# Performance work log

Measured on AMD Instinct MI355X. Metric: run time of the kernel, lower is better.

The kernel has to match this reference:

```python
import jax, jax.numpy as jnp
import numpy as np

EPS = 1e-5  # torch LayerNorm default
H, DH = 8, 64  # heads, dim_head


def _ln(x, g, b):
    mu = jnp.mean(x, axis=-1, keepdims=True)
    var = jnp.var(x, axis=-1, keepdims=True)
    return (x - mu) / jnp.sqrt(var + EPS) * g + b


def setup_inputs() -> dict:
    key = jax.random.key(0)
    ks = jax.random.split(key, 8)
    B, N, M, D, CD = 4, 2048, 256, 1024, 768
    J = M + 1 + N  # context + null + self
    return {
        "x": jax.random.normal(ks[0], (B, N, D), jnp.float32),
        "context": jax.random.normal(ks[1], (B, M, CD), jnp.float32),
        "att_bias": jax.random.normal(ks[2], (B, H, N, J), jnp.float32) * 0.02,
        "ln_g": jnp.ones((D,), jnp.float32),
        "ln_b": jnp.zeros((D,), jnp.float32),
        "null_kv": jax.random.normal(ks[3], (2, DH), jnp.float32),
        "Wq": jax.random.normal(ks[4], (D, H * DH), jnp.float32) * 0.02,
        "Wkv": jax.random.normal(ks[5], (D, 2 * DH), jnp.float32) * 0.02,
        "cln_g": jnp.ones((CD,), jnp.float32),
        "cln_b": jnp.zeros((CD,), jnp.float32),
        "Wc": jax.random.normal(ks[6], (CD, 2 * DH), jnp.float32) * 0.02,
        "bc": jnp.zeros((2 * DH,), jnp.float32),
        "Wo": jax.random.normal(ks[7], (H * DH, D), jnp.float32) * 0.02,
        "oln_g": jnp.ones((D,), jnp.float32),
        "oln_b": jnp.zeros((D,), jnp.float32),
    }


def reference(x, context, att_bias, ln_g, ln_b, null_kv, Wq, Wkv,
              cln_g, cln_b, Wc, bc, Wo, oln_g, oln_b):
    B, N, D = x.shape
    scale = DH ** -0.5
    xn = _ln(x, ln_g, ln_b)
    # queries: per-head [b,h,n,dh], pre-scaled
    q = (xn @ Wq).reshape(B, N, H, DH).transpose(0, 2, 1, 3) * scale
    # shared single-head k/v [b,n,dh]
    kv = xn @ Wkv
    k, v = kv[..., :DH], kv[..., DH:]
    # context k/v [b,m,dh]
    ckv = _ln(context, cln_g, cln_b) @ Wc + bc
    ck, cv = ckv[..., :DH], ckv[..., DH:]
    # null kv token [b,1,dh]
    nk = jnp.broadcast_to(null_kv[0], (B, 1, DH))
    nv = jnp.broadcast_to(null_kv[1], (B, 1, DH))
    # torch order: cat null first, then context -> (ck, nk, k)
    k = jnp.concatenate([ck, nk, k], axis=1)  # [b, j, dh]
    v = jnp.concatenate([cv, nv, v], axis=1)
    score = jnp.einsum('bhid,bjd->bhij', q, k) + att_bias
    probs = jax.nn.softmax(score.astype(jnp.float32), axis=-1).astype(v.dtype)
    att = jnp.einsum('bhij,bjd->bhid', probs, v)
    att = att.transpose(0, 2, 1, 3).reshape(B, N, H * DH)
    return _ln(att @ Wo, oln_g, oln_b)
```

## Files before the change

### kernel.cpp

```cpp
#include <hip/hip_runtime.h>
#include <hip/hip_bf16.h>
#include <cstdint>
#include <cstddef>

#define Bq  4
#define Nq  2048
#define Mq  256
#define Dq  1024
#define CDq 768
#define Hq  8
#define DHq 64
#define Jq  2305
#define QKVN 640
#define NCH 37
#define J2  (NCH * 64)

typedef __bf16  bf16x8 __attribute__((ext_vector_type(8)));
typedef float   f32x4  __attribute__((ext_vector_type(4)));
typedef short   s16x8  __attribute__((ext_vector_type(8)));
typedef unsigned short u16;
typedef unsigned int   u32;

__device__ __forceinline__ u16 f2b(float v) {
  unsigned x = __builtin_bit_cast(unsigned, v);
  unsigned r = (x + 0x7fffu + ((x >> 16) & 1u)) >> 16;
  return (u16)r;
}
__device__ __forceinline__ float b2f(u16 u) {
  unsigned x = ((unsigned)u) << 16;
  return __builtin_bit_cast(float, x);
}
__device__ __forceinline__ u32 cvtpk(float lo, float hi) {
  u32 r;
  asm("v_cvt_pk_bf16_f32 %0, %1, %2" : "=v"(r) : "v"(lo), "v"(hi));
  return r;
}
__device__ __forceinline__ f32x4 mfma16(bf16x8 a, bf16x8 b, f32x4 c) {
  return __builtin_amdgcn_mfma_f32_16x16x32_bf16(a, b, c, 0, 0, 0);
}
__device__ __forceinline__ bf16x8 frag_ld(const u16* p) {
  return __builtin_bit_cast(bf16x8, *(const s16x8*)p);
}
__device__ __forceinline__ void stout(float* p, float v) { *p = v; }
__device__ __forceinline__ void stout(u16*   p, float v) { *p = f2b(v); }

__device__ __forceinline__ void gl_lds16(const void* gSrc, void* ldsDst) {
  __builtin_amdgcn_global_load_lds(
      (const __attribute__((address_space(1))) void*)gSrc,
      (__attribute__((address_space(3))) void*)ldsDst, 16, 0, 0);
}

__global__ __launch_bounds__(256) void prep_kernel(
    const float* __restrict__ x,   const float* __restrict__ ln_g,
    const float* __restrict__ ln_b, u16* __restrict__ xn,
    const float* __restrict__ ctx, const float* __restrict__ cln_g,
    const float* __restrict__ cln_b, u16* __restrict__ ctxn,
    const float* __restrict__ Wq, const float* __restrict__ Wkv,
    const float* __restrict__ Wc, const float* __restrict__ Wo,
    u16* __restrict__ WqkvT, u16* __restrict__ WcT, u16* __restrict__ WoT) {
  const int tid = threadIdx.x;
  if (blockIdx.x < Bq * Nq + Bq * Mq) {
    const int row = blockIdx.x;
    const float* in; const float* g; const float* bb; u16* out; int D;
    if (row < Bq * Nq) {
      in = x + (size_t)row * Dq; g = ln_g; bb = ln_b;
      out = xn + (size_t)row * Dq; D = Dq;
    } else {
      int r2 = row - Bq * Nq;
      in = ctx + (size_t)r2 * CDq; g = cln_g; bb = cln_b;
      out = ctxn + (size_t)r2 * CDq; D = CDq;
    }
    __shared__ float buf[1024];
    __shared__ float red[8];
    float s = 0.f, s2 = 0.f;
    for (int i = tid; i < D; i += 256) {
      float v = in[i];
      buf[i] = v;
      s += v; s2 += v * v;
    }
    #pragma unroll
    for (int off = 32; off; off >>= 1) {
      s  += __shfl_down(s,  off);
      s2 += __shfl_down(s2, off);
    }
    if ((tid & 63) == 0) { red[tid >> 6] = s; red[4 + (tid >> 6)] = s2; }
    __syncthreads();
    float sum = red[0] + red[1] + red[2] + red[3];
    float sq  = red[4] + red[5] + red[6] + red[7];
    float mean = sum / D;
    float var  = sq / D - mean * mean;
    float rstd = rsqrtf(var + 1e-5f);
    for (int i = tid; i < D; i += 256)
      out[i] = f2b((buf[i] - mean) * rstd * g[i] + bb[i]);
  } else {
    __shared__ float T[32][33];
    int bid = blockIdx.x - (Bq * Nq + Bq * Mq);
    const float* W; u16* WT; int K, N, bx, by;
    if (bid < 512)      { W = Wq;  WT = WqkvT;                    K = 1024; N = 512;  bx = bid % 16;        by = bid / 16; }
    else if (bid < 640) { W = Wkv; WT = WqkvT + (size_t)512*1024; K = 1024; N = 128;  bx = (bid-512) % 4;   by = (bid-512) / 4; }
    else if (bid < 736) { W = Wc;  WT = WcT;                      K = 768;  N = 128;  bx = (bid-640) % 4;   by = (bid-640) / 4; }
    else                { W = Wo;  WT = WoT;                      K = 512;  N = 1024; bx = (bid-736) % 32;  by = (bid-736) / 32; }
    const int n0 = bx * 32, k0 = by * 32;
    const int tx = tid & 31, ty = tid >> 5;
    #pragma unroll
    for (int i = 0; i < 32; i += 8)
      T[ty + i][tx] = W[(size_t)(k0 + ty + i) * N + n0 + tx];
    __syncthreads();
    #pragma unroll
    for (int i = 0; i < 32; i += 8)
      WT[(size_t)(n0 + ty + i) * K + k0 + tx] = f2b(T[tx][ty + i]);
  }
}

__global__ __launch_bounds__(256) void ln_out_kernel(
    const float* __restrict__ in, const float* __restrict__ g,
    const float* __restrict__ bb, float* __restrict__ out) {
  const int row = blockIdx.x;
  const int tid = threadIdx.x;
  __shared__ float buf[1024];
  __shared__ float red[8];
  const float* xr = in + (size_t)row * Dq;
  float s = 0.f, s2 = 0.f;
  for (int i = tid; i < Dq; i += 256) {
    float v = xr[i];
    buf[i] = v;
    s += v; s2 += v * v;
  }
  #pragma unroll
  for (int off = 32; off; off >>= 1) {
    s  += __shfl_down(s,  off);
    s2 += __shfl_down(s2, off);
  }
  if ((tid & 63) == 0) { red[tid >> 6] = s; red[4 + (tid >> 6)] = s2; }
  __syncthreads();
  float sum = red[0] + red[1] + red[2] + red[3];
  float sq  = red[4] + red[5] + red[6] + red[7];
  float mean = sum / Dq;
  float var  = sq / Dq - mean * mean;
  float rstd = rsqrtf(var + 1e-5f);
  for (int i = tid; i < Dq; i += 256)
    out[(size_t)row * Dq + i] = (buf[i] - mean) * rstd * g[i] + bb[i];
}

template <typename OT>
__device__ __forceinline__ void gemm_body(const u16* __restrict__ A,
                                          const u16* __restrict__ BT,
                                          OT* __restrict__ C,
                                          int N, int K, int m0, int n0,
                                          u16* Al, u16* Bl) {
  const int tid  = threadIdx.x;
  const int lane = tid & 63, wave = tid >> 6;
  const int l16  = lane & 15, lhi = lane >> 4;
  const int wm = (wave >> 1) * 64, wn = (wave & 1) * 64;

  const int offB = (wave << 10) + (lane << 4);
  const int srow = offB >> 6;
  const int scby = offB & 63;

  f32x4 acc[4][4];
  #pragma unroll
  for (int i = 0; i < 4; ++i)
    #pragma unroll
    for (int j = 0; j < 4; ++j) acc[i][j] = f32x4{0.f, 0.f, 0.f, 0.f};

  for (int k0 = 0; k0 < K; k0 += 32) {
    __syncthreads();
    #pragma unroll
    for (int c = 0; c < 2; ++c) {
      gl_lds16((const char*)(A  + (size_t)(m0 + srow + c * 64) * K + k0) + scby,
               (char*)Al + c * 4096 + (wave << 10));
      gl_lds16((const char*)(BT + (size_t)(n0 + srow + c * 64) * K + k0) + scby,
               (char*)Bl + c * 4096 + (wave << 10));
    }
    __syncthreads();

    bf16x8 af[4], bfr[4];
    #pragma unroll
    for (int mt = 0; mt < 4; ++mt)
      af[mt] = frag_ld(Al + (wm + mt * 16 + l16) * 32 + lhi * 8);
    #pragma unroll
    for (int nt = 0; nt < 4; ++nt)
      bfr[nt] = frag_ld(Bl + (wn + nt * 16 + l16) * 32 + lhi * 8);
    __builtin_amdgcn_s_setprio(1);
    #pragma unroll
    for (int mt = 0; mt < 4; ++mt)
      #pragma unroll
      for (int nt = 0; nt < 4; ++nt)
        acc[mt][nt] = mfma16(af[mt], bfr[nt], acc[mt][nt]);
    __builtin_amdgcn_s_setprio(0);
  }

  #pragma unroll
  for (int mt = 0; mt < 4; ++mt)
    #pragma unroll
    for (int nt = 0; nt < 4; ++nt)
      #pragma unroll
      for (int r = 0; r < 4; ++r)
        stout(C + (size_t)(m0 + wm + mt * 16 + lhi * 4 + r) * N
                + (n0 + wn + nt * 16 + l16),
              acc[mt][nt][r]);
}

__global__ __launch_bounds__(256) void gemm_qkv_ckv(
    const u16* __restrict__ xn, const u16* __restrict__ WqkvT,
    u16* __restrict__ qkv,
    const u16* __restrict__ ctxn, const u16* __restrict__ WcT,
    u16* __restrict__ ckvb) {
  const u16 *A, *BT; u16* C; int N, K, m0, n0;
  if (blockIdx.y < 5) {
    A = xn; BT = WqkvT; C = qkv; N = QKVN; K = Dq;
    m0 = blockIdx.x * 128; n0 = blockIdx.y * 128;
  } else {
    if (blockIdx.x >= 8) return;
    A = ctxn; BT = WcT; C = ckvb; N = 2 * DHq; K = CDq;
    m0 = blockIdx.x * 128; n0 = 0;
  }
  __shared__ __align__(16) u16 Al[128 * 32];
  __shared__ __align__(16) u16 Bl[128 * 32];
  gemm_body<u16>(A, BT, C, N, K, m0, n0, Al, Bl);
}

__global__ __launch_bounds__(256) void gemm128f(const u16* __restrict__ A,
                                                const u16* __restrict__ BT,
                                                float* __restrict__ C,
                                                int N, int K) {
  __shared__ __align__(16) u16 Al[128 * 32];
  __shared__ __align__(16) u16 Bl[128 * 32];
  gemm_body<float>(A, BT, C, N, K, blockIdx.x * 128, blockIdx.y * 128, Al, Bl);
}

__global__ void build_kv(const u16* __restrict__ qkv,
                         const u16* __restrict__ ckvb,
                         const float* __restrict__ nullkv,
                         const float* __restrict__ bc,
                         u16* __restrict__ Kt, u16* __restrict__ Vt) {
  int idx = blockIdx.x * 256 + threadIdx.x;
  if (idx >= Bq * J2 * 64) return;
  int d = idx & 63;
  int t = idx >> 6;
  int j = t % J2;
  int b = t / J2;
  float k = 0.f, v = 0.f;
  if (j < Mq) {
    const u16* p = ckvb + (size_t)(b * Mq + j) * 128;
    k = b2f(p[d])      + bc[d];
    v = b2f(p[64 + d]) + bc[64 + d];
  } else if (j == Mq) {
    k = nullkv[d];
    v = nullkv[64 + d];
  } else if (j < Jq) {
    const u16* p = qkv + (size_t)(b * Nq + (j - Mq - 1)) * QKVN + 512;
    k = b2f(p[d]);
    v = b2f(p[64 + d]);
  }
  int ch = j >> 6, row = j & 63;
  char* tbase = (char*)Kt + ((size_t)(b * NCH + ch)) * 8192;
  *(u16*)(tbase + row * 128 + ((d << 1) ^ ((row & 7) << 4))) = f2b(k);
  char* vbase = (char*)Vt + ((size_t)(b * NCH + ch)) * 8192;
  *(u16*)(vbase + d * 128 + ((row << 1) ^ ((d & 7) << 4))) = f2b(v);
}

__global__ __launch_bounds__(256, 4) void attn_kernel(
    const u16* __restrict__ qkv, const u16* __restrict__ Kt,
    const u16* __restrict__ Vt, const float* __restrict__ bias,
    u16* __restrict__ att) {
  __shared__ __align__(16) u16 Kl [2][4096];
  __shared__ __align__(16) u16 VTl[2][4096];
  __shared__ __align__(16) u16 Pl [4][16][64];
  const int tid  = threadIdx.x;
  const int wave = tid >> 6, lane = tid & 63;
  const int l16  = lane & 15, lhi = lane >> 4;
  const int qt = blockIdx.x, h = blockIdx.y, b = blockIdx.z;
  const int qrow0 = qt * 64 + wave * 16;

  bf16x8 qf[2];
  {
    const u16* qp = qkv + ((size_t)(b * Nq + qrow0 + l16)) * QKVN
                        + h * DHq + lhi * 8;
    qf[0] = frag_ld(qp);
    qf[1] = frag_ld(qp + 32);
  }

  float m_s = -INFINITY, l_s = 0.f;
  f32x4 oacc[4];
  #pragma unroll
  for (int dt = 0; dt < 4; ++dt) oacc[dt] = f32x4{0.f, 0.f, 0.f, 0.f};

  const float* bptr = bias
      + ((size_t)((b * Hq + h) * (size_t)Nq + qrow0 + l16)) * Jq + 4 * lhi;

  const size_t tb0 = (size_t)b * NCH;
  const int soff = (wave << 10) + (lane << 4);
  char* plw = (char*)&Pl[wave][0][0];
  const int pmask = (l16 & 7) << 4;

  auto stage = [&](int buf, int ch) {
    const char* kt = (const char*)Kt + (tb0 + ch) * 8192 + soff;
    const char* vt = (const char*)Vt + (tb0 + ch) * 8192 + soff;
    char* kl = (char*)&Kl[buf][0]  + (wave << 10);
    char* vl = (char*)&VTl[buf][0] + (wave << 10);
    gl_lds16(kt,        kl);
    gl_lds16(kt + 4096, kl + 4096);
    gl_lds16(vt,        vl);
    gl_lds16(vt + 4096, vl + 4096);
  };

  auto loadBias = [&](float (&bv)[4][4], int ch) {
    const int jc = ch * 64;
    if (ch < NCH - 1) {
      #pragma unroll
      for (int jt = 0; jt < 4; ++jt)
        #pragma unroll
        for (int r = 0; r < 4; ++r)
          bv[jt][r] = bptr[jc + 16 * jt + r];
    } else {
      #pragma unroll
      for (int jt = 0; jt < 4; ++jt)
        #pragma unroll
        for (int r = 0; r < 4; ++r) {
          int jg = jc + 16 * jt + 4 * lhi + r;
          bv[jt][r] = (jg < Jq) ? bptr[jc + 16 * jt + r] : -1e30f;
        }
    }
  };

  float bvA[4][4], bvB[4][4];
  stage(0, 0);
  loadBias(bvA, 0);
  __syncthreads();

  auto body = [&](int ch, float (&bvC)[4][4], float (&bvN)[4][4]) {
    const int cur = ch & 1;
    if (ch + 1 < NCH) {
      stage(cur ^ 1, ch + 1);
      loadBias(bvN, ch + 1);
    }

    float sv[4][4];
    __builtin_amdgcn_s_setprio(1);
    #pragma unroll
    for (int jt = 0; jt < 4; ++jt) {
      const int krow = jt * 16 + l16;
      const char* kb = (const char*)&Kl[cur][0] + krow * 128;
      const int sw = (krow & 7) << 4;
      f32x4 s = f32x4{0.f, 0.f, 0.f, 0.f};
      s = mfma16(frag_ld((const u16*)(kb + (((lhi << 4))      ^ sw))), qf[0], s);
      s = mfma16(frag_ld((const u16*)(kb + ((64 + (lhi << 4)) ^ sw))), qf[1], s);
      #pragma unroll
      for (int r = 0; r < 4; ++r)
        sv[jt][r] = s[r] * 0.125f + bvC[jt][r];
    }
    __builtin_amdgcn_s_setprio(0);

    float pmax = sv[0][0];
    #pragma unroll
    for (int jt = 0; jt < 4; ++jt)
      #pragma unroll
      for (int r = 0; r < 4; ++r) pmax = fmaxf(pmax, sv[jt][r]);
    pmax = fmaxf(pmax, __shfl_xor(pmax, 16));
    pmax = fmaxf(pmax, __shfl_xor(pmax, 32));

    if (__any(pmax > m_s + 8.f)) {
      float mnew = fmaxf(m_s, pmax);
      float corr = __expf(m_s - mnew);
      l_s *= corr;
      m_s = mnew;
      #pragma unroll
      for (int r = 0; r < 4; ++r) {
        float c = __shfl(corr, lhi * 4 + r);
        #pragma unroll
        for (int dt = 0; dt < 4; ++dt) oacc[dt][r] *= c;
      }
    }

    float ps = 0.f;
    #pragma unroll
    for (int jt = 0; jt < 4; ++jt)
      #pragma unroll
      for (int r = 0; r < 4; ++r) {
        float pv = __expf(sv[jt][r] - m_s);
        sv[jt][r] = pv;
        ps += pv;
      }
    ps += __shfl_xor(ps, 16);
    ps += __shfl_xor(ps, 32);
    l_s += ps;

    #pragma unroll
    for (int jt = 0; jt < 4; ++jt) {
      const int c = 32 * jt + 8 * lhi;
      *(u32*)(plw + l16 * 128 + ((c)     ^ pmask)) = cvtpk(sv[jt][0], sv[jt][1]);
      *(u32*)(plw + l16 * 128 + ((c + 4) ^ pmask)) = cvtpk(sv[jt][2], sv[jt][3]);
    }

    #pragma unroll
    for (int jk = 0; jk < 2; ++jk) {
      bf16x8 pf = frag_ld((const u16*)(plw + l16 * 128
                                       + ((jk * 64 + lhi * 16) ^ pmask)));
      __builtin_amdgcn_s_setprio(1);
      #pragma unroll
      for (int dt = 0; dt < 4; ++dt) {
        const int vrow = dt * 16 + l16;
        const char* vb = (const char*)&VTl[cur][0] + vrow * 128;
        bf16x8 vf = frag_ld((const u16*)(vb + ((jk * 64 + (lhi << 4)) ^ ((vrow & 7) << 4))));
        oacc[dt] = mfma16(pf, vf, oacc[dt]);
      }
      __builtin_amdgcn_s_setprio(0);
    }
    __syncthreads();
  };

  int ch = 0;
  while (true) {
    body(ch, bvA, bvB);
    if (++ch == NCH) break;
    body(ch, bvB, bvA);
    if (++ch == NCH) break;
  }

  float linv = 1.0f / l_s;
  #pragma unroll
  for (int r = 0; r < 4; ++r) {
    float inv = __shfl(linv, lhi * 4 + r);
    int row = qrow0 + lhi * 4 + r;
    u16* op = att + ((size_t)(b * Nq + row)) * (Hq * DHq) + h * DHq;
    #pragma unroll
    for (int dt = 0; dt < 4; ++dt)
      op[dt * 16 + l16] = f2b(oacc[dt][r] * inv);
  }
}

extern "C" void kernel_launch(void* const* d_in, const int* in_sizes, int n_in,
                              void* d_out, int out_size, void* d_ws, size_t ws_size,
                              hipStream_t stream) {
  const float* x       = (const float*)d_in[0];
  const float* context = (const float*)d_in[1];
  const float* att_bias= (const float*)d_in[2];
  const float* ln_g    = (const float*)d_in[3];
  const float* ln_b    = (const float*)d_in[4];
  const float* null_kv = (const float*)d_in[5];
  const float* Wq      = (const float*)d_in[6];
  const float* Wkv     = (const float*)d_in[7];
  const float* cln_g   = (const float*)d_in[8];
  const float* cln_b   = (const float*)d_in[9];
  const float* Wc      = (const float*)d_in[10];
  const float* bc      = (const float*)d_in[11];
  const float* Wo      = (const float*)d_in[12];
  const float* oln_g   = (const float*)d_in[13];
  const float* oln_b   = (const float*)d_in[14];
  float* out = (float*)d_out;

  char* p = (char*)d_ws;
  auto alloc = [&](size_t bytes) {
    void* r = (void*)p;
    p += (bytes + 255) & ~(size_t)255;
    return r;
  };
  u16* xn     = (u16*)alloc((size_t)Bq * Nq * Dq * 2);
  u16* ctxn   = (u16*)alloc((size_t)Bq * Mq * CDq * 2);
  u16* WqkvT  = (u16*)alloc((size_t)QKVN * Dq * 2);
  u16* WcT    = (u16*)alloc((size_t)2 * DHq * CDq * 2);
  u16* WoT    = (u16*)alloc((size_t)Dq * Hq * DHq * 2);
  u16* qkv    = (u16*)alloc((size_t)Bq * Nq * QKVN * 2);
  u16* ckvb   = (u16*)alloc((size_t)Bq * Mq * 2 * DHq * 2);
  u16* Ktil   = (u16*)alloc((size_t)Bq * NCH * 8192);
  u16* Vtil   = (u16*)alloc((size_t)Bq * NCH * 8192);
  u16* attb   = (u16*)alloc((size_t)Bq * Nq * Hq * DHq * 2);
  float* y    = (float*)alloc((size_t)Bq * Nq * Dq * 4);

  prep_kernel<<<Bq * Nq + Bq * Mq + 1248, 256, 0, stream>>>(
      x, ln_g, ln_b, xn, context, cln_g, cln_b, ctxn,
      Wq, Wkv, Wc, Wo, WqkvT, WcT, WoT);

  gemm_qkv_ckv<<<dim3(Bq * Nq / 128, 6), 256, 0, stream>>>(
      xn, WqkvT, qkv, ctxn, WcT, ckvb);

  build_kv<<<(Bq * J2 * 64 + 255) / 256, 256, 0, stream>>>(
      qkv, ckvb, null_kv, bc, Ktil, Vtil);

  attn_kernel<<<dim3(Nq / 64, Hq, Bq), 256, 0, stream>>>(
      qkv, Ktil, Vtil, att_bias, attb);

  gemm128f<<<dim3(Bq * Nq / 128, Dq / 128), 256, 0, stream>>>(
      attb, WoT, y, Dq, Hq * DHq);
  ln_out_kernel<<<Bq * Nq, 256, 0, stream>>>(y, oln_g, oln_b, out);
}
```

Before: 271.6 us.

## Switch attention to 32x32 MFMA tiles with register-resident P via permlane swap

Restructures the attention kernel to use 32x32x16 bf16 MFMA with two waves of 32 query rows each, instead of four waves of 16 rows using 16x16 MFMA. The probability tile no longer round-trips through LDS: packed bf16 values are rearranged between lanes with v_permlane32_swap to form the A operand directly. Bias loads become vectorized 4-float loads issued after the score computation. This cuts LDS traffic and the instruction count per tile, at the cost of fewer waves per block, higher register pressure from the 16-wide accumulators, and less latency hiding.

After: 261.7 us. 3.6% less time.

```diff
diff --git a/kernel.cpp b/kernel.cpp
--- a/kernel.cpp
+++ b/kernel.cpp
@@ -17,7 +17,10 @@
 
 typedef __bf16  bf16x8 __attribute__((ext_vector_type(8)));
 typedef float   f32x4  __attribute__((ext_vector_type(4)));
+typedef float   f32x4u __attribute__((ext_vector_type(4), aligned(4)));
+typedef float   f32x16 __attribute__((ext_vector_type(16)));
 typedef short   s16x8  __attribute__((ext_vector_type(8)));
+typedef unsigned int u32x4 __attribute__((ext_vector_type(4)));
 typedef unsigned short u16;
 typedef unsigned int   u32;
 
@@ -35,8 +38,14 @@
   asm("v_cvt_pk_bf16_f32 %0, %1, %2" : "=v"(r) : "v"(lo), "v"(hi));
   return r;
 }
+__device__ __forceinline__ void pswap(u32& a, u32& b) {
+  asm volatile("v_permlane32_swap_b32 %0, %1" : "+v"(a), "+v"(b));
+}
 __device__ __forceinline__ f32x4 mfma16(bf16x8 a, bf16x8 b, f32x4 c) {
   return __builtin_amdgcn_mfma_f32_16x16x32_bf16(a, b, c, 0, 0, 0);
+}
+__device__ __forceinline__ f32x16 mfma32(bf16x8 a, bf16x8 b, f32x16 c) {
+  return __builtin_amdgcn_mfma_f32_32x32x16_bf16(a, b, c, 0, 0, 0);
 }
 __device__ __forceinline__ bf16x8 frag_ld(const u16* p) {
   return __builtin_bit_cast(bf16x8, *(const s16x8*)p);
@@ -260,104 +269,115 @@
   *(u16*)(vbase + d * 128 + ((row << 1) ^ ((d & 7) << 4))) = f2b(v);
 }
 
-__global__ __launch_bounds__(256, 4) void attn_kernel(
+__global__ __launch_bounds__(128) void attn_kernel(
     const u16* __restrict__ qkv, const u16* __restrict__ Kt,
     const u16* __restrict__ Vt, const float* __restrict__ bias,
     u16* __restrict__ att) {
   __shared__ __align__(16) u16 Kl [2][4096];
   __shared__ __align__(16) u16 VTl[2][4096];
-  __shared__ __align__(16) u16 Pl [4][16][64];
   const int tid  = threadIdx.x;
   const int wave = tid >> 6, lane = tid & 63;
-  const int l16  = lane & 15, lhi = lane >> 4;
+  const int l = lane & 31, hi = lane >> 5;
   const int qt = blockIdx.x, h = blockIdx.y, b = blockIdx.z;
-  const int qrow0 = qt * 64 + wave * 16;
-
-  bf16x8 qf[2];
+  const int qrow0 = qt * 64 + wave * 32;
+
+  bf16x8 qf[4];
   {
-    const u16* qp = qkv + ((size_t)(b * Nq + qrow0 + l16)) * QKVN
-                        + h * DHq + lhi * 8;
-    qf[0] = frag_ld(qp);
-    qf[1] = frag_ld(qp + 32);
+    const u16* qp = qkv + ((size_t)(b * Nq + qrow0 + l)) * QKVN
+                        + h * DHq + hi * 8;
+    #pragma unroll
+    for (int kt = 0; kt < 4; ++kt) qf[kt] = frag_ld(qp + kt * 16);
   }
 
   float m_s = -INFINITY, l_s = 0.f;
-  f32x4 oacc[4];
+  f32x16 oacc[2];
   #pragma unroll
-  for (int dt = 0; dt < 4; ++dt) oacc[dt] = f32x4{0.f, 0.f, 0.f, 0.f};
-
-  const float* bptr = bias
-      + ((size_t)((b * Hq + h) * (size_t)Nq + qrow0 + l16)) * Jq + 4 * lhi;
+  for (int dt = 0; dt < 2; ++dt)
+    #pragma unroll
+    for (int r = 0; r < 16; ++r) oacc[dt][r] = 0.f;
+
+  const float* bp = bias
+      + ((size_t)((b * Hq + h) * (size_t)Nq + qrow0 + l)) * Jq + 4 * hi;
 
   const size_t tb0 = (size_t)b * NCH;
-  const int soff = (wave << 10) + (lane << 4);
-  char* plw = (char*)&Pl[wave][0][0];
-  const int pmask = (l16 & 7) << 4;
+  const int soff = (wave << 12) + (lane << 4);
 
   auto stage = [&](int buf, int ch) {
-    const char* kt = (const char*)Kt + (tb0 + ch) * 8192 + soff;
-    const char* vt = (const char*)Vt + (tb0 + ch) * 8192 + soff;
-    char* kl = (char*)&Kl[buf][0]  + (wave << 10);
-    char* vl = (char*)&VTl[buf][0] + (wave << 10);
-    gl_lds16(kt,        kl);
-    gl_lds16(kt + 4096, kl + 4096);
-    gl_lds16(vt,        vl);
-    gl_lds16(vt + 4096, vl + 4096);
+    const char* kt_ = (const char*)Kt + (tb0 + ch) * 8192 + soff;
+    const char* vt_ = (const char*)Vt + (tb0 + ch) * 8192 + soff;
+    char* kl = (char*)&Kl[buf][0]  + (wave << 12);
+    char* vl = (char*)&VTl[buf][0] + (wave << 12);
+    #pragma unroll
+    for (int i = 0; i < 4; ++i) {
+      gl_lds16(kt_ + i * 1024, kl + i * 1024);
+      gl_lds16(vt_ + i * 1024, vl + i * 1024);
+    }
   };
 
-  auto loadBias = [&](float (&bv)[4][4], int ch) {
+  f32x4 bv[2][4];
+  auto loadBias = [&](int ch) {
     const int jc = ch * 64;
     if (ch < NCH - 1) {
       #pragma unroll
-      for (int jt = 0; jt < 4; ++jt)
+      for (int jt = 0; jt < 2; ++jt)
         #pragma unroll
-        for (int r = 0; r < 4; ++r)
-          bv[jt][r] = bptr[jc + 16 * jt + r];
+        for (int g = 0; g < 4; ++g)
+          bv[jt][g] = (f32x4)(*(const f32x4u*)(bp + jc + jt * 32 + 8 * g));
     } else {
       #pragma unroll
-      for (int jt = 0; jt < 4; ++jt)
+      for (int jt = 0; jt < 2; ++jt)
         #pragma unroll
-        for (int r = 0; r < 4; ++r) {
-          int jg = jc + 16 * jt + 4 * lhi + r;
-          bv[jt][r] = (jg < Jq) ? bptr[jc + 16 * jt + r] : -1e30f;
-        }
+        for (int g = 0; g < 4; ++g)
+          #pragma unroll
+          for (int e = 0; e < 4; ++e) {
+            int jg = jc + jt * 32 + 8 * g + 4 * hi + e;
+            bv[jt][g][e] = (jg < Jq) ? bp[jc + jt * 32 + 8 * g + e] : -1e30f;
+          }
     }
   };
 
-  float bvA[4][4], bvB[4][4];
   stage(0, 0);
-  loadBias(bvA, 0);
+  loadBias(0);
   __syncthreads();
 
-  auto body = [&](int ch, float (&bvC)[4][4], float (&bvN)[4][4]) {
+  for (int ch = 0; ch < NCH; ++ch) {
     const int cur = ch & 1;
-    if (ch + 1 < NCH) {
-      stage(cur ^ 1, ch + 1);
-      loadBias(bvN, ch + 1);
-    }
-
-    float sv[4][4];
+    if (ch + 1 < NCH) stage(cur ^ 1, ch + 1);
+    const char* kbase = (const char*)&Kl[cur][0];
+    const char* vbase = (const char*)&VTl[cur][0];
+
+    f32x16 sacc[2];
+    #pragma unroll
+    for (int jt = 0; jt < 2; ++jt)
+      #pragma unroll
+      for (int r = 0; r < 16; ++r) sacc[jt][r] = 0.f;
     __builtin_amdgcn_s_setprio(1);
     #pragma unroll
-    for (int jt = 0; jt < 4; ++jt) {
-      const int krow = jt * 16 + l16;
-      const char* kb = (const char*)&Kl[cur][0] + krow * 128;
-      const int sw = (krow & 7) << 4;
-      f32x4 s = f32x4{0.f, 0.f, 0.f, 0.f};
-      s = mfma16(frag_ld((const u16*)(kb + (((lhi << 4))      ^ sw))), qf[0], s);
-      s = mfma16(frag_ld((const u16*)(kb + ((64 + (lhi << 4)) ^ sw))), qf[1], s);
-      #pragma unroll
-      for (int r = 0; r < 4; ++r)
-        sv[jt][r] = s[r] * 0.125f + bvC[jt][r];
+    for (int jt = 0; jt < 2; ++jt) {
+      const int row = jt * 32 + l;
+      const int sw = (row & 7) << 4;
+      #pragma unroll
+      for (int kt = 0; kt < 4; ++kt) {
+        bf16x8 kf = frag_ld((const u16*)(kbase + row * 128
+                                         + ((kt * 32 + hi * 16) ^ sw)));
+        sacc[jt] = mfma32(kf, qf[kt], sacc[jt]);
+      }
     }
     __builtin_amdgcn_s_setprio(0);
 
+    float sv[2][16];
+    #pragma unroll
+    for (int jt = 0; jt < 2; ++jt)
+      #pragma unroll
+      for (int r = 0; r < 16; ++r)
+        sv[jt][r] = sacc[jt][r] * 0.125f + bv[jt][r >> 2][r & 3];
+    if (ch + 1 < NCH) loadBias(ch + 1);
+
     float pmax = sv[0][0];
     #pragma unroll
-    for (int jt = 0; jt < 4; ++jt)
-      #pragma unroll
-      for (int r = 0; r < 4; ++r) pmax = fmaxf(pmax, sv[jt][r]);
-    pmax = fmaxf(pmax, __shfl_xor(pmax, 16));
+    for (int jt = 0; jt < 2; ++jt)
+      #pragma unroll
+      for (int r = 0; r < 16; ++r) pmax = fmaxf(pmax, sv[jt][r]);
     pmax = fmaxf(pmax, __shfl_xor(pmax, 32));
 
     if (__any(pmax > m_s + 8.f)) {
@@ -366,67 +386,63 @@
       l_s *= corr;
       m_s = mnew;
       #pragma unroll
-      for (int r = 0; r < 4; ++r) {
-        float c = __shfl(corr, lhi * 4 + r);
-        #pragma unroll
-        for (int dt = 0; dt < 4; ++dt) oacc[dt][r] *= c;
+      for (int r = 0; r < 16; ++r) {
+        float c = __shfl(corr, (r & 3) + 8 * (r >> 2) + 4 * hi);
+        oacc[0][r] *= c;
+        oacc[1][r] *= c;
       }
     }
 
     float ps = 0.f;
     #pragma unroll
-    for (int jt = 0; jt < 4; ++jt)
-      #pragma unroll
-      for (int r = 0; r < 4; ++r) {
+    for (int jt = 0; jt < 2; ++jt)
+      #pragma unroll
+      for (int r = 0; r < 16; ++r) {
         float pv = __expf(sv[jt][r] - m_s);
         sv[jt][r] = pv;
         ps += pv;
       }
-    ps += __shfl_xor(ps, 16);
     ps += __shfl_xor(ps, 32);
     l_s += ps;
 
-    #pragma unroll
-    for (int jt = 0; jt < 4; ++jt) {
-      const int c = 32 * jt + 8 * lhi;
-      *(u32*)(plw + l16 * 128 + ((c)     ^ pmask)) = cvtpk(sv[jt][0], sv[jt][1]);
-      *(u32*)(plw + l16 * 128 + ((c + 4) ^ pmask)) = cvtpk(sv[jt][2], sv[jt][3]);
-    }
-
-    #pragma unroll
-    for (int jk = 0; jk < 2; ++jk) {
-      bf16x8 pf = frag_ld((const u16*)(plw + l16 * 128
-                                       + ((jk * 64 + lhi * 16) ^ pmask)));
+    u32 pk[2][8];
+    #pragma unroll
+    for (int jt = 0; jt < 2; ++jt)
+      #pragma unroll
+      for (int g = 0; g < 4; ++g) {
+        pk[jt][2 * g]     = cvtpk(sv[jt][4 * g],     sv[jt][4 * g + 1]);
+        pk[jt][2 * g + 1] = cvtpk(sv[jt][4 * g + 2], sv[jt][4 * g + 3]);
+      }
+
+    #pragma unroll
+    for (int kt = 0; kt < 4; ++kt) {
+      const int t = kt & 1, js = kt >> 1;
+      u32 a0 = pk[js][4 * t],     b0 = pk[js][4 * t + 2];
+      u32 a1 = pk[js][4 * t + 1], b1 = pk[js][4 * t + 3];
+      pswap(a0, b0);
+      pswap(a1, b1);
+      bf16x8 paf = __builtin_bit_cast(bf16x8, u32x4{a0, a1, b0, b1});
       __builtin_amdgcn_s_setprio(1);
       #pragma unroll
-      for (int dt = 0; dt < 4; ++dt) {
-        const int vrow = dt * 16 + l16;
-        const char* vb = (const char*)&VTl[cur][0] + vrow * 128;
-        bf16x8 vf = frag_ld((const u16*)(vb + ((jk * 64 + (lhi << 4)) ^ ((vrow & 7) << 4))));
-        oacc[dt] = mfma16(pf, vf, oacc[dt]);
+      for (int dt = 0; dt < 2; ++dt) {
+        const int vrow = dt * 32 + l;
+        bf16x8 vf = frag_ld((const u16*)(vbase + vrow * 128
+                     + ((kt * 32 + hi * 16) ^ ((vrow & 7) << 4))));
+        oacc[dt] = mfma32(paf, vf, oacc[dt]);
       }
       __builtin_amdgcn_s_setprio(0);
     }
     __syncthreads();
-  };
-
-  int ch = 0;
-  while (true) {
-    body(ch, bvA, bvB);
-    if (++ch == NCH) break;
-    body(ch, bvB, bvA);
-    if (++ch == NCH) break;
   }
 
   float linv = 1.0f / l_s;
   #pragma unroll
-  for (int r = 0; r < 4; ++r) {
-    float inv = __shfl(linv, lhi * 4 + r);
-    int row = qrow0 + lhi * 4 + r;
-    u16* op = att + ((size_t)(b * Nq + row)) * (Hq * DHq) + h * DHq;
-    #pragma unroll
-    for (int dt = 0; dt < 4; ++dt)
-      op[dt * 16 + l16] = f2b(oacc[dt][r] * inv);
+  for (int r = 0; r < 16; ++r) {
+    const int qo = (r & 3) + 8 * (r >> 2) + 4 * hi;
+    float inv = __shfl(linv, qo);
+    u16* op = att + ((size_t)(b * Nq + qrow0 + qo)) * (Hq * DHq) + h * DHq + l;
+    op[0]  = f2b(oacc[0][r] * inv);
+    op[32] = f2b(oacc[1][r] * inv);
   }
 }
 
@@ -478,7 +494,7 @@
   build_kv<<<(Bq * J2 * 64 + 255) / 256, 256, 0, stream>>>(
       qkv, ckvb, null_kv, bc, Ktil, Vtil);
 
-  attn_kernel<<<dim3(Nq / 64, Hq, Bq), 256, 0, stream>>>(
+  attn_kernel<<<dim3(Nq / 64, Hq, Bq), 128, 0, stream>>>(
       qkv, Ktil, Vtil, att_bias, attb);
 
   gemm128f<<<dim3(Bq * Nq / 128, Dq / 128), 256, 0, stream>>>(
```

## Double attention key chunk to 128, vectorize bias loads, store output projection as bf16

Applied to the files above, without the earlier changes.

The attention kernel now processes keys in 128-wide chunks (19 chunks instead of 37), doubling the LDS tiles for K, V and P and loading the bias as 4-wide vectors. The goal is to halve per-chunk overhead: barriers, softmax max/rescale checks and staging setup. The occupancy hint of 4 blocks per CU is dropped because LDS use per block roughly doubles. Separately, the output projection GEMM writes bf16 instead of fp32 and the final LayerNorm reads bf16 with vector loads, which halves that intermediate traffic at some precision cost before normalization.

After: 253.2 us. 6.8% less time.

```diff
diff --git a/kernel.cpp b/kernel.cpp
--- a/kernel.cpp
+++ b/kernel.cpp
@@ -12,12 +12,14 @@
 #define DHq 64
 #define Jq  2305
 #define QKVN 640
-#define NCH 37
-#define J2  (NCH * 64)
+#define NCH 19
+#define J2  (NCH * 128)
 
 typedef __bf16  bf16x8 __attribute__((ext_vector_type(8)));
 typedef float   f32x4  __attribute__((ext_vector_type(4)));
+typedef float   f32x4u __attribute__((ext_vector_type(4), aligned(4)));
 typedef short   s16x8  __attribute__((ext_vector_type(8)));
+typedef short   s16x4  __attribute__((ext_vector_type(4)));
 typedef unsigned short u16;
 typedef unsigned int   u32;
 
@@ -113,18 +115,22 @@
 }
 
 __global__ __launch_bounds__(256) void ln_out_kernel(
-    const float* __restrict__ in, const float* __restrict__ g,
+    const u16* __restrict__ in, const float* __restrict__ g,
     const float* __restrict__ bb, float* __restrict__ out) {
   const int row = blockIdx.x;
   const int tid = threadIdx.x;
   __shared__ float buf[1024];
   __shared__ float red[8];
-  const float* xr = in + (size_t)row * Dq;
+  const u16* xr = in + (size_t)row * Dq;
   float s = 0.f, s2 = 0.f;
-  for (int i = tid; i < Dq; i += 256) {
-    float v = xr[i];
-    buf[i] = v;
-    s += v; s2 += v * v;
+  {
+    s16x4 v4 = *(const s16x4*)(xr + tid * 4);
+    #pragma unroll
+    for (int e = 0; e < 4; ++e) {
+      float v = b2f((u16)v4[e]);
+      buf[tid * 4 + e] = v;
+      s += v; s2 += v * v;
+    }
   }
   #pragma unroll
   for (int off = 32; off; off >>= 1) {
@@ -138,8 +144,11 @@
   float mean = sum / Dq;
   float var  = sq / Dq - mean * mean;
   float rstd = rsqrtf(var + 1e-5f);
-  for (int i = tid; i < Dq; i += 256)
+  #pragma unroll
+  for (int e = 0; e < 4; ++e) {
+    int i = tid * 4 + e;
     out[(size_t)row * Dq + i] = (buf[i] - mean) * rstd * g[i] + bb[i];
+  }
 }
 
 template <typename OT>
@@ -220,13 +229,13 @@
   gemm_body<u16>(A, BT, C, N, K, m0, n0, Al, Bl);
 }
 
-__global__ __launch_bounds__(256) void gemm128f(const u16* __restrict__ A,
+__global__ __launch_bounds__(256) void gemm128b(const u16* __restrict__ A,
                                                 const u16* __restrict__ BT,
-                                                float* __restrict__ C,
+                                                u16* __restrict__ C,
                                                 int N, int K) {
   __shared__ __align__(16) u16 Al[128 * 32];
   __shared__ __align__(16) u16 Bl[128 * 32];
-  gemm_body<float>(A, BT, C, N, K, blockIdx.x * 128, blockIdx.y * 128, Al, Bl);
+  gemm_body<u16>(A, BT, C, N, K, blockIdx.x * 128, blockIdx.y * 128, Al, Bl);
 }
 
 __global__ void build_kv(const u16* __restrict__ qkv,
@@ -253,20 +262,20 @@
     k = b2f(p[d]);
     v = b2f(p[64 + d]);
   }
-  int ch = j >> 6, row = j & 63;
-  char* tbase = (char*)Kt + ((size_t)(b * NCH + ch)) * 8192;
+  int ch = j >> 7, row = j & 127;
+  char* tbase = (char*)Kt + ((size_t)(b * NCH + ch)) * 16384;
   *(u16*)(tbase + row * 128 + ((d << 1) ^ ((row & 7) << 4))) = f2b(k);
-  char* vbase = (char*)Vt + ((size_t)(b * NCH + ch)) * 8192;
-  *(u16*)(vbase + d * 128 + ((row << 1) ^ ((d & 7) << 4))) = f2b(v);
-}
-
-__global__ __launch_bounds__(256, 4) void attn_kernel(
+  char* vbase = (char*)Vt + ((size_t)(b * NCH + ch)) * 16384;
+  *(u16*)(vbase + d * 256 + ((row << 1) ^ ((d & 7) << 4))) = f2b(v);
+}
+
+__global__ __launch_bounds__(256) void attn_kernel(
     const u16* __restrict__ qkv, const u16* __restrict__ Kt,
     const u16* __restrict__ Vt, const float* __restrict__ bias,
     u16* __restrict__ att) {
-  __shared__ __align__(16) u16 Kl [2][4096];
-  __shared__ __align__(16) u16 VTl[2][4096];
-  __shared__ __align__(16) u16 Pl [4][16][64];
+  __shared__ __align__(16) u16 Kl [2][8192];
+  __shared__ __align__(16) u16 VTl[2][8192];
+  __shared__ __align__(16) u16 Pl [4][16][128];
   const int tid  = threadIdx.x;
   const int wave = tid >> 6, lane = tid & 63;
   const int l16  = lane & 15, lhi = lane >> 4;
@@ -290,58 +299,59 @@
       + ((size_t)((b * Hq + h) * (size_t)Nq + qrow0 + l16)) * Jq + 4 * lhi;
 
   const size_t tb0 = (size_t)b * NCH;
-  const int soff = (wave << 10) + (lane << 4);
+  const int soff = (wave << 12) + (lane << 4);
   char* plw = (char*)&Pl[wave][0][0];
   const int pmask = (l16 & 7) << 4;
 
   auto stage = [&](int buf, int ch) {
-    const char* kt = (const char*)Kt + (tb0 + ch) * 8192 + soff;
-    const char* vt = (const char*)Vt + (tb0 + ch) * 8192 + soff;
-    char* kl = (char*)&Kl[buf][0]  + (wave << 10);
-    char* vl = (char*)&VTl[buf][0] + (wave << 10);
-    gl_lds16(kt,        kl);
-    gl_lds16(kt + 4096, kl + 4096);
-    gl_lds16(vt,        vl);
-    gl_lds16(vt + 4096, vl + 4096);
+    const char* kt_ = (const char*)Kt + (tb0 + ch) * 16384 + soff;
+    const char* vt_ = (const char*)Vt + (tb0 + ch) * 16384 + soff;
+    char* kl = (char*)&Kl[buf][0]  + (wave << 12);
+    char* vl = (char*)&VTl[buf][0] + (wave << 12);
+    #pragma unroll
+    for (int i = 0; i < 4; ++i) {
+      gl_lds16(kt_ + i * 1024, kl + i * 1024);
+      gl_lds16(vt_ + i * 1024, vl + i * 1024);
+    }
   };
 
-  auto loadBias = [&](float (&bv)[4][4], int ch) {
-    const int jc = ch * 64;
+  auto loadBias = [&](f32x4 (&bv)[8], int ch) {
+    const int jc = ch * 128;
     if (ch < NCH - 1) {
       #pragma unroll
-      for (int jt = 0; jt < 4; ++jt)
+      for (int jt = 0; jt < 8; ++jt)
+        bv[jt] = (f32x4)(*(const f32x4u*)(bptr + jc + 16 * jt));
+    } else {
+      #pragma unroll
+      for (int jt = 0; jt < 8; ++jt)
         #pragma unroll
-        for (int r = 0; r < 4; ++r)
-          bv[jt][r] = bptr[jc + 16 * jt + r];
-    } else {
-      #pragma unroll
-      for (int jt = 0; jt < 4; ++jt)
-        #pragma unroll
-        for (int r = 0; r < 4; ++r) {
-          int jg = jc + 16 * jt + 4 * lhi + r;
-          bv[jt][r] = (jg < Jq) ? bptr[jc + 16 * jt + r] : -1e30f;
+        for (int e = 0; e < 4; ++e) {
+          int jg = jc + 16 * jt + 4 * lhi + e;
+          bv[jt][e] = (jg < Jq) ? bptr[jc + 16 * jt + e] : -1e30f;
         }
     }
   };
 
-  float bvA[4][4], bvB[4][4];
+  f32x4 bvA[8], bvB[8];
   stage(0, 0);
   loadBias(bvA, 0);
   __syncthreads();
 
-  auto body = [&](int ch, float (&bvC)[4][4], float (&bvN)[4][4]) {
+  auto body = [&](int ch, f32x4 (&bvC)[8], f32x4 (&bvN)[8]) {
     const int cur = ch & 1;
     if (ch + 1 < NCH) {
       stage(cur ^ 1, ch + 1);
       loadBias(bvN, ch + 1);
     }
-
-    float sv[4][4];
+    const char* kbase = (const char*)&Kl[cur][0];
+    const char* vbase = (const char*)&VTl[cur][0];
+
+    float sv[8][4];
     __builtin_amdgcn_s_setprio(1);
     #pragma unroll
-    for (int jt = 0; jt < 4; ++jt) {
+    for (int jt = 0; jt < 8; ++jt) {
       const int krow = jt * 16 + l16;
-      const char* kb = (const char*)&Kl[cur][0] + krow * 128;
+      const char* kb = kbase + krow * 128;
       const int sw = (krow & 7) << 4;
       f32x4 s = f32x4{0.f, 0.f, 0.f, 0.f};
       s = mfma16(frag_ld((const u16*)(kb + (((lhi << 4))      ^ sw))), qf[0], s);
@@ -354,7 +364,7 @@
 
     float pmax = sv[0][0];
     #pragma unroll
-    for (int jt = 0; jt < 4; ++jt)
+    for (int jt = 0; jt < 8; ++jt)
       #pragma unroll
       for (int r = 0; r < 4; ++r) pmax = fmaxf(pmax, sv[jt][r]);
     pmax = fmaxf(pmax, __shfl_xor(pmax, 16));
@@ -375,7 +385,7 @@
 
     float ps = 0.f;
     #pragma unroll
-    for (int jt = 0; jt < 4; ++jt)
+    for (int jt = 0; jt < 8; ++jt)
       #pragma unroll
       for (int r = 0; r < 4; ++r) {
         float pv = __expf(sv[jt][r] - m_s);
@@ -387,22 +397,22 @@
     l_s += ps;
 
     #pragma unroll
-    for (int jt = 0; jt < 4; ++jt) {
+    for (int jt = 0; jt < 8; ++jt) {
       const int c = 32 * jt + 8 * lhi;
-      *(u32*)(plw + l16 * 128 + ((c)     ^ pmask)) = cvtpk(sv[jt][0], sv[jt][1]);
-      *(u32*)(plw + l16 * 128 + ((c + 4) ^ pmask)) = cvtpk(sv[jt][2], sv[jt][3]);
-    }
-
-    #pragma unroll
-    for (int jk = 0; jk < 2; ++jk) {
-      bf16x8 pf = frag_ld((const u16*)(plw + l16 * 128
+      *(u32*)(plw + l16 * 256 + ((c)     ^ pmask)) = cvtpk(sv[jt][0], sv[jt][1]);
+      *(u32*)(plw + l16 * 256 + ((c + 4) ^ pmask)) = cvtpk(sv[jt][2], sv[jt][3]);
+    }
+
+    #pragma unroll
+    for (int jk = 0; jk < 4; ++jk) {
+      bf16x8 pf = frag_ld((const u16*)(plw + l16 * 256
                                        + ((jk * 64 + lhi * 16) ^ pmask)));
       __builtin_amdgcn_s_setprio(1);
       #pragma unroll
       for (int dt = 0; dt < 4; ++dt) {
         const int vrow = dt * 16 + l16;
-        const char* vb = (const char*)&VTl[cur][0] + vrow * 128;
-        bf16x8 vf = frag_ld((const u16*)(vb + ((jk * 64 + (lhi << 4)) ^ ((vrow & 7) << 4))));
+        bf16x8 vf = frag_ld((const u16*)(vbase + vrow * 256
+                     + ((jk * 64 + (lhi << 4)) ^ ((vrow & 7) << 4))));
         oacc[dt] = mfma16(pf, vf, oacc[dt]);
       }
       __builtin_amdgcn_s_setprio(0);
@@ -463,10 +473,10 @@
   u16* WoT    = (u16*)alloc((size_t)Dq * Hq * DHq * 2);
   u16* qkv    = (u16*)alloc((size_t)Bq * Nq * QKVN * 2);
   u16* ckvb   = (u16*)alloc((size_t)Bq * Mq * 2 * DHq * 2);
-  u16* Ktil   = (u16*)alloc((size_t)Bq * NCH * 8192);
-  u16* Vtil   = (u16*)alloc((size_t)Bq * NCH * 8192);
+  u16* Ktil   = (u16*)alloc((size_t)Bq * NCH * 16384);
+  u16* Vtil   = (u16*)alloc((size_t)Bq * NCH * 16384);
   u16* attb   = (u16*)alloc((size_t)Bq * Nq * Hq * DHq * 2);
-  float* y    = (float*)alloc((size_t)Bq * Nq * Dq * 4);
+  u16* y      = (u16*)alloc((size_t)Bq * Nq * Dq * 2);
 
   prep_kernel<<<Bq * Nq + Bq * Mq + 1248, 256, 0, stream>>>(
       x, ln_g, ln_b, xn, context, cln_g, cln_b, ctxn,
@@ -481,7 +491,7 @@
   attn_kernel<<<dim3(Nq / 64, Hq, Bq), 256, 0, stream>>>(
       qkv, Ktil, Vtil, att_bias, attb);
 
-  gemm128f<<<dim3(Bq * Nq / 128, Dq / 128), 256, 0, stream>>>(
+  gemm128b<<<dim3(Bq * Nq / 128, Dq / 128), 256, 0, stream>>>(
       attb, WoT, y, Dq, Hq * DHq);
   ln_out_kernel<<<Bq * Nq, 256, 0, stream>>>(y, oln_g, oln_b, out);
 }
```

## Share K/V tiles across all heads per block and store out-proj in bf16

Applied to the files above, without the earlier changes.

The attention kernel now launches 512-thread blocks where each of the 8 waves handles one head for the same 16 query rows. Every K/V chunk staged in shared memory is therefore reused by all heads, since K/V is shared across heads, instead of being reloaded once per head block. Bias loads are vectorised to 16-byte reads. Separately, the output-projection GEMM writes bf16 instead of fp32 and the final LayerNorm reads bf16 with vector loads, which halves that intermediate traffic at some precision cost before normalisation.

After: 253.9 us. 1.07x faster.

```diff
diff --git a/kernel.cpp b/kernel.cpp
--- a/kernel.cpp
+++ b/kernel.cpp
@@ -17,7 +17,9 @@
 
 typedef __bf16  bf16x8 __attribute__((ext_vector_type(8)));
 typedef float   f32x4  __attribute__((ext_vector_type(4)));
+typedef float   f32x4u __attribute__((ext_vector_type(4), aligned(4)));
 typedef short   s16x8  __attribute__((ext_vector_type(8)));
+typedef short   s16x4  __attribute__((ext_vector_type(4)));
 typedef unsigned short u16;
 typedef unsigned int   u32;
 
@@ -113,18 +115,22 @@
 }
 
 __global__ __launch_bounds__(256) void ln_out_kernel(
-    const float* __restrict__ in, const float* __restrict__ g,
+    const u16* __restrict__ in, const float* __restrict__ g,
     const float* __restrict__ bb, float* __restrict__ out) {
   const int row = blockIdx.x;
   const int tid = threadIdx.x;
   __shared__ float buf[1024];
   __shared__ float red[8];
-  const float* xr = in + (size_t)row * Dq;
+  const u16* xr = in + (size_t)row * Dq;
   float s = 0.f, s2 = 0.f;
-  for (int i = tid; i < Dq; i += 256) {
-    float v = xr[i];
-    buf[i] = v;
-    s += v; s2 += v * v;
+  {
+    s16x4 v4 = *(const s16x4*)(xr + tid * 4);
+    #pragma unroll
+    for (int e = 0; e < 4; ++e) {
+      float v = b2f((u16)v4[e]);
+      buf[tid * 4 + e] = v;
+      s += v; s2 += v * v;
+    }
   }
   #pragma unroll
   for (int off = 32; off; off >>= 1) {
@@ -138,8 +144,11 @@
   float mean = sum / Dq;
   float var  = sq / Dq - mean * mean;
   float rstd = rsqrtf(var + 1e-5f);
-  for (int i = tid; i < Dq; i += 256)
+  #pragma unroll
+  for (int e = 0; e < 4; ++e) {
+    int i = tid * 4 + e;
     out[(size_t)row * Dq + i] = (buf[i] - mean) * rstd * g[i] + bb[i];
+  }
 }
 
 template <typename OT>
@@ -220,13 +229,13 @@
   gemm_body<u16>(A, BT, C, N, K, m0, n0, Al, Bl);
 }
 
-__global__ __launch_bounds__(256) void gemm128f(const u16* __restrict__ A,
+__global__ __launch_bounds__(256) void gemm128b(const u16* __restrict__ A,
                                                 const u16* __restrict__ BT,
-                                                float* __restrict__ C,
+                                                u16* __restrict__ C,
                                                 int N, int K) {
   __shared__ __align__(16) u16 Al[128 * 32];
   __shared__ __align__(16) u16 Bl[128 * 32];
-  gemm_body<float>(A, BT, C, N, K, blockIdx.x * 128, blockIdx.y * 128, Al, Bl);
+  gemm_body<u16>(A, BT, C, N, K, blockIdx.x * 128, blockIdx.y * 128, Al, Bl);
 }
 
 __global__ void build_kv(const u16* __restrict__ qkv,
@@ -260,18 +269,19 @@
   *(u16*)(vbase + d * 128 + ((row << 1) ^ ((d & 7) << 4))) = f2b(v);
 }
 
-__global__ __launch_bounds__(256, 4) void attn_kernel(
+__global__ __launch_bounds__(512, 4) void attn_kernel(
     const u16* __restrict__ qkv, const u16* __restrict__ Kt,
     const u16* __restrict__ Vt, const float* __restrict__ bias,
     u16* __restrict__ att) {
   __shared__ __align__(16) u16 Kl [2][4096];
   __shared__ __align__(16) u16 VTl[2][4096];
-  __shared__ __align__(16) u16 Pl [4][16][64];
+  __shared__ __align__(16) u16 Pl [8][16][64];
   const int tid  = threadIdx.x;
   const int wave = tid >> 6, lane = tid & 63;
   const int l16  = lane & 15, lhi = lane >> 4;
-  const int qt = blockIdx.x, h = blockIdx.y, b = blockIdx.z;
-  const int qrow0 = qt * 64 + wave * 16;
+  const int qt = blockIdx.x, b = blockIdx.z;
+  const int h = wave;
+  const int qrow0 = qt * 16;
 
   bf16x8 qf[2];
   {
@@ -295,53 +305,49 @@
   const int pmask = (l16 & 7) << 4;
 
   auto stage = [&](int buf, int ch) {
-    const char* kt = (const char*)Kt + (tb0 + ch) * 8192 + soff;
-    const char* vt = (const char*)Vt + (tb0 + ch) * 8192 + soff;
-    char* kl = (char*)&Kl[buf][0]  + (wave << 10);
-    char* vl = (char*)&VTl[buf][0] + (wave << 10);
-    gl_lds16(kt,        kl);
-    gl_lds16(kt + 4096, kl + 4096);
-    gl_lds16(vt,        vl);
-    gl_lds16(vt + 4096, vl + 4096);
+    const char* kt_ = (const char*)Kt + (tb0 + ch) * 8192 + soff;
+    const char* vt_ = (const char*)Vt + (tb0 + ch) * 8192 + soff;
+    gl_lds16(kt_, (char*)&Kl[buf][0]  + (wave << 10));
+    gl_lds16(vt_, (char*)&VTl[buf][0] + (wave << 10));
   };
 
-  auto loadBias = [&](float (&bv)[4][4], int ch) {
+  auto loadBias = [&](f32x4 (&bv)[4], int ch) {
     const int jc = ch * 64;
     if (ch < NCH - 1) {
       #pragma unroll
       for (int jt = 0; jt < 4; ++jt)
-        #pragma unroll
-        for (int r = 0; r < 4; ++r)
-          bv[jt][r] = bptr[jc + 16 * jt + r];
+        bv[jt] = (f32x4)(*(const f32x4u*)(bptr + jc + 16 * jt));
     } else {
       #pragma unroll
       for (int jt = 0; jt < 4; ++jt)
         #pragma unroll
-        for (int r = 0; r < 4; ++r) {
-          int jg = jc + 16 * jt + 4 * lhi + r;
-          bv[jt][r] = (jg < Jq) ? bptr[jc + 16 * jt + r] : -1e30f;
+        for (int e = 0; e < 4; ++e) {
+          int jg = jc + 16 * jt + 4 * lhi + e;
+          bv[jt][e] = (jg < Jq) ? bptr[jc + 16 * jt + e] : -1e30f;
         }
     }
   };
 
-  float bvA[4][4], bvB[4][4];
+  f32x4 bvA[4], bvB[4];
   stage(0, 0);
   loadBias(bvA, 0);
   __syncthreads();
 
-  auto body = [&](int ch, float (&bvC)[4][4], float (&bvN)[4][4]) {
+  auto body = [&](int ch, f32x4 (&bvC)[4], f32x4 (&bvN)[4]) {
     const int cur = ch & 1;
     if (ch + 1 < NCH) {
       stage(cur ^ 1, ch + 1);
       loadBias(bvN, ch + 1);
     }
+    const char* kbase = (const char*)&Kl[cur][0];
+    const char* vbase = (const char*)&VTl[cur][0];
 
     float sv[4][4];
     __builtin_amdgcn_s_setprio(1);
     #pragma unroll
     for (int jt = 0; jt < 4; ++jt) {
       const int krow = jt * 16 + l16;
-      const char* kb = (const char*)&Kl[cur][0] + krow * 128;
+      const char* kb = kbase + krow * 128;
       const int sw = (krow & 7) << 4;
       f32x4 s = f32x4{0.f, 0.f, 0.f, 0.f};
       s = mfma16(frag_ld((const u16*)(kb + (((lhi << 4))      ^ sw))), qf[0], s);
@@ -401,8 +407,8 @@
       #pragma unroll
       for (int dt = 0; dt < 4; ++dt) {
         const int vrow = dt * 16 + l16;
-        const char* vb = (const char*)&VTl[cur][0] + vrow * 128;
-        bf16x8 vf = frag_ld((const u16*)(vb + ((jk * 64 + (lhi << 4)) ^ ((vrow & 7) << 4))));
+        bf16x8 vf = frag_ld((const u16*)(vbase + vrow * 128
+                     + ((jk * 64 + (lhi << 4)) ^ ((vrow & 7) << 4))));
         oacc[dt] = mfma16(pf, vf, oacc[dt]);
       }
       __builtin_amdgcn_s_setprio(0);
@@ -466,7 +472,7 @@
   u16* Ktil   = (u16*)alloc((size_t)Bq * NCH * 8192);
   u16* Vtil   = (u16*)alloc((size_t)Bq * NCH * 8192);
   u16* attb   = (u16*)alloc((size_t)Bq * Nq * Hq * DHq * 2);
-  float* y    = (float*)alloc((size_t)Bq * Nq * Dq * 4);
+  u16* y      = (u16*)alloc((size_t)Bq * Nq * Dq * 2);
 
   prep_kernel<<<Bq * Nq + Bq * Mq + 1248, 256, 0, stream>>>(
       x, ln_g, ln_b, xn, context, cln_g, cln_b, ctxn,
@@ -478,10 +484,10 @@
   build_kv<<<(Bq * J2 * 64 + 255) / 256, 256, 0, stream>>>(
       qkv, ckvb, null_kv, bc, Ktil, Vtil);
 
-  attn_kernel<<<dim3(Nq / 64, Hq, Bq), 256, 0, stream>>>(
+  attn_kernel<<<dim3(Nq / 16, 1, Bq), 512, 0, stream>>>(
       qkv, Ktil, Vtil, att_bias, attb);
 
-  gemm128f<<<dim3(Bq * Nq / 128, Dq / 128), 256, 0, stream>>>(
+  gemm128b<<<dim3(Bq * Nq / 128, Dq / 128), 256, 0, stream>>>(
       attb, WoT, y, Dq, Hq * DHq);
   ln_out_kernel<<<Bq * Nq, 256, 0, stream>>>(y, oln_g, oln_b, out);
 }
```
